# Optimization experiments

Measured on AMD Instinct MI355X. Metric: run time of the kernel, lower is better.

The kernel has to match this reference:

```python
import jax, jax.numpy as jnp
import numpy as np

C64 = jnp.complex64

# ---- gate matrices (PennyLane conventions) ----

def u3(theta, phi, delta):
    ct, st = jnp.cos(theta / 2), jnp.sin(theta / 2)
    return jnp.stack([
        jnp.stack([ct + 0j, -jnp.exp(1j * delta) * st]),
        jnp.stack([jnp.exp(1j * phi) * st, jnp.exp(1j * (phi + delta)) * ct]),
    ]).astype(C64)

def ising_zz(t):
    em, ep = jnp.exp(-1j * t / 2), jnp.exp(1j * t / 2)
    return jnp.diag(jnp.stack([em, ep, ep, em])).astype(C64)

_XX = np.fliplr(np.eye(4)).astype(np.complex64)
_YY = np.array([[0, 0, 0, -1], [0, 0, 1, 0], [0, 1, 0, 0], [-1, 0, 0, 0]], np.complex64)
_I4 = np.eye(4, dtype=np.complex64)

def ising_xx(t):
    return (jnp.cos(t / 2) * _I4 - 1j * jnp.sin(t / 2) * _XX).astype(C64)

def ising_yy(t):
    return (jnp.cos(t / 2) * _I4 - 1j * jnp.sin(t / 2) * _YY).astype(C64)

def crot(phi, theta, omega):
    # controlled-Rot(phi,theta,omega); control = first wire of apply_2q
    ct, st = jnp.cos(theta / 2), jnp.sin(theta / 2)
    r = jnp.stack([
        jnp.stack([jnp.exp(-1j * (phi + omega) / 2) * ct, -jnp.exp(1j * (phi - omega) / 2) * st]),
        jnp.stack([jnp.exp(-1j * (phi - omega) / 2) * st, jnp.exp(1j * (phi + omega) / 2) * ct]),
    ])
    U = jnp.eye(4, dtype=C64)
    return U.at[2:, 2:].set(r.astype(C64))

# ---- statevector gate application; state shape (S, 2, 2, ..., 2) (wire 0 = axis 1) ----

def apply_1q(state, U, q):
    st = jnp.tensordot(U, state, axes=[[1], [q + 1]])  # (2, S, ...)
    return jnp.moveaxis(st, 0, q + 1)

def apply_2q(state, U4, q1, q2):
    Ut = U4.reshape(2, 2, 2, 2)  # (o1, o2, i1, i2)
    st = jnp.tensordot(Ut, state, axes=[[2, 3], [q1 + 1, q2 + 1]])
    return jnp.moveaxis(st, [0, 1], [q1 + 1, q2 + 1])

KERNEL, DILATION = 8, 1

def setup_inputs() -> dict:
    key = jax.random.key(0)
    ks = jax.random.split(key, 5)
    B, C, T = 16, 32, 128
    nq, depth = 10, 3
    return {
        "x": jax.random.normal(ks[0], (B, C, T), jnp.float32),
        "fc_w": jax.random.normal(ks[1], (nq, C * KERNEL), jnp.float32) * (1.0 / np.sqrt(C * KERNEL)),
        "fc_b": jax.random.normal(ks[2], (nq,), jnp.float32) * 0.01,
        "conv_params": jax.random.normal(ks[3], (depth, nq, 15), jnp.float32),
        "pool_params": jax.random.normal(ks[4], (depth, nq // 2, 3), jnp.float32),
    }

def reference(x, fc_w, fc_b, conv_params, pool_params):
    B, C, T = x.shape
    nq = fc_w.shape[0]
    k = fc_w.shape[1] // C
    depth = conv_params.shape[0]
    d = DILATION
    n_win = T - (k - 1) * d

    # temporal windows -> classical embedding (angles)
    idx = jnp.arange(n_win)[:, None] + d * jnp.arange(k)[None, :]  # (n_win, k)
    win = x[:, :, idx]                                             # (B, C, n_win, k)
    flat = jnp.transpose(win, (0, 2, 1, 3)).reshape(B, n_win, C * k)
    angles = (jnp.einsum('bwf,ef->bwe', flat, fc_w) + fc_b).reshape(-1, nq)  # (S, nq)
    S = angles.shape[0]

    # AngleEmbedding with RY on |0...0> gives a product state
    half = angles / 2
    c, s = jnp.cos(half), jnp.sin(half)
    state = jnp.ones((S, 1), C64)
    for q in range(nq):
        qubit = jnp.stack([c[:, q], s[:, q]], axis=-1).astype(C64)  # (S, 2)
        state = (state[:, :, None] * qubit[:, None, :]).reshape(S, -1)
    state = state.reshape((S,) + (2,) * nq)

    wires = list(range(nq))
    for layer in range(depth):
        W = conv_params[layer]
        P = pool_params[layer]
        nw = len(wires)
        # convolution: U3 pairs + IsingZZ/YY/XX + U3 pairs, even then odd brickwork
        for p in (0, 1):
            for indx in range(nw - 1):
                if indx % 2 == p:
                    w1, w2 = wires[indx], wires[indx + 1]
                    state = apply_1q(state, u3(*W[indx, 0:3]), w1)
                    state = apply_1q(state, u3(*W[indx + 1, 3:6]), w2)
                    state = apply_2q(state, ising_zz(W[indx, 6]), w1, w2)
                    state = apply_2q(state, ising_yy(W[indx, 7]), w1, w2)
                    state = apply_2q(state, ising_xx(W[indx, 8]), w1, w2)
                    state = apply_1q(state, u3(*W[indx, 9:12]), w1)
                    state = apply_1q(state, u3(*W[indx + 1, 12:15]), w2)
        # pooling: CRot from discarded (odd) wire onto kept (even) wire
        for j in range(nw // 2):
            ctrl, tgt = wires[2 * j + 1], wires[2 * j]
            state = apply_2q(state, crot(*P[j]), ctrl, tgt)
        wires = wires[::2]

    # expval(PauliZ(0))
    probs = state.real ** 2 + state.imag ** 2
    p01 = probs.reshape(S, 2, -1).sum(-1)  # marginal over wire 0
    z = p01[:, 0] - p01[:, 1]
    return z.reshape(B, n_win)
```

## Files before the change

kernel.cpp:

```cpp
#include <hip/hip_runtime.h>

#define NWIN 121
#define NQ 10
#define NGATES 23
#define WPB 4

typedef float v2f __attribute__((ext_vector_type(2)));

__device__ static const int dGT[NGATES] = {0,0,0,0,0,0,0,0,0, 1,1,1,1,1, 0,0,0,0, 1,1, 0,0, 1};
__device__ static const int dGL[NGATES] = {0,0,0,0,0,0,0,0,0, 0,0,0,0,0, 1,1,1,1, 1,1, 2,2, 2};
__device__ static const int dGP[NGATES] = {0,2,4,6,8,1,3,5,7, 0,1,2,3,4, 0,2,1,3, 0,1, 0,1, 0};

__host__ __device__ constexpr int REGB[4][4] = {
    {5,6,7,8},{1,2,3,4},{0,1,3,5},{3,5,7,9}};
__host__ __device__ constexpr int LANEB[4][6] = {
    {0,1,2,3,4,9},{0,5,6,7,8,9},{2,4,6,7,8,9},{0,1,2,4,6,8}};

__host__ __device__ constexpr int hswz(int p, int L){
    return p==0 ? ((((L>>5)&1)<<1)|(((L>>6)&1)<<2)|(((L>>7)&1)<<3))
         : p==1 ? (((L>>4)&1) | ((((L>>5)&1)^((L>>6)&1))<<1) | (((L>>7)&1)<<2) | (((L>>8)&1)<<3))
         :        (((L>>4)&1) | (((L>>6)&1)<<1) | (((L>>8)&1)<<3));
}
__host__ __device__ constexpr int offsL(int ph, int r){
    int o = 0;
    for (int k=0;k<4;++k) if ((r>>k)&1) o |= 1<<REGB[ph][k];
    return o;
}

struct cpx { float x, y; };
__device__ __forceinline__ cpx cmul(cpx a, cpx b){ return {a.x*b.x - a.y*b.y, a.x*b.y + a.y*b.x}; }
__device__ __forceinline__ cpx cadd(cpx a, cpx b){ return {a.x+b.x, a.y+b.y}; }
__device__ __forceinline__ cpx cscale(float s, cpx a){ return {s*a.x, s*a.y}; }
__device__ __forceinline__ cpx cexp_i(float t){ return {cosf(t), sinf(t)}; }
__device__ __forceinline__ cpx mulnegi(cpx z){ return {z.y, -z.x}; }
__device__ __forceinline__ cpx csel(int c, cpx a, cpx b){ return {c ? a.x : b.x, c ? a.y : b.y}; }

__device__ __forceinline__ void u3m(cpx A[2][2], float th, float ph, float de){
    float ct = cosf(0.5f*th), st = sinf(0.5f*th);
    cpx ed  = cexp_i(de);
    cpx ep  = cexp_i(ph);
    cpx epd = cexp_i(ph + de);
    A[0][0] = {ct, 0.f};
    A[0][1] = {-ed.x*st, -ed.y*st};
    A[1][0] = { ep.x*st,  ep.y*st};
    A[1][1] = { epd.x*ct, epd.y*ct};
}

__device__ __forceinline__ void build_gate_col(int g, int c,
                                               const float* __restrict__ conv,
                                               const float* __restrict__ pool,
                                               cpx (&Mc)[4])
{
    int l = dGL[g], pi = dGP[g];
    if (dGT[g] == 0) {
        const float* W1 = conv + l*150 + pi*15;
        const float* W2 = conv + l*150 + (pi+1)*15;
        cpx A1[2][2], B1[2][2], A2[2][2], B2[2][2];
        u3m(A1, W1[0],  W1[1],  W1[2]);
        u3m(B1, W2[3],  W2[4],  W2[5]);
        u3m(A2, W1[9],  W1[10], W1[11]);
        u3m(B2, W2[12], W2[13], W2[14]);
        const int c1 = c >> 1, c2 = c & 1;
        cpx a1r0 = csel(c1, A1[0][1], A1[0][0]);
        cpx a1r1 = csel(c1, A1[1][1], A1[1][0]);
        cpx b1r0 = csel(c2, B1[0][1], B1[0][0]);
        cpx b1r1 = csel(c2, B1[1][1], B1[1][0]);
        cpx T[4];
        T[0] = cmul(a1r0, b1r0);
        T[1] = cmul(a1r0, b1r1);
        T[2] = cmul(a1r1, b1r0);
        T[3] = cmul(a1r1, b1r1);
        float tz = W1[6];
        cpx em = cexp_i(-0.5f*tz), ep = cexp_i(0.5f*tz);
        T[0] = cmul(em, T[0]); T[1] = cmul(ep, T[1]);
        T[2] = cmul(ep, T[2]); T[3] = cmul(em, T[3]);
        float ty = W1[7]; float cy = cosf(0.5f*ty), sy = sinf(0.5f*ty);
        cpx T2_[4];
        T2_[0] = cadd(cscale(cy,T[0]), mulnegi(cscale(-sy, T[3])));
        T2_[1] = cadd(cscale(cy,T[1]), mulnegi(cscale( sy, T[2])));
        T2_[2] = cadd(cscale(cy,T[2]), mulnegi(cscale( sy, T[1])));
        T2_[3] = cadd(cscale(cy,T[3]), mulnegi(cscale(-sy, T[0])));
        float tx = W1[8]; float cx = cosf(0.5f*tx), sx = sinf(0.5f*tx);
        cpx T3_[4];
        T3_[0] = cadd(cscale(cx,T2_[0]), mulnegi(cscale(sx, T2_[3])));
        T3_[1] = cadd(cscale(cx,T2_[1]), mulnegi(cscale(sx, T2_[2])));
        T3_[2] = cadd(cscale(cx,T2_[2]), mulnegi(cscale(sx, T2_[1])));
        T3_[3] = cadd(cscale(cx,T2_[3]), mulnegi(cscale(sx, T2_[0])));
        cpx K2[4][4];
        #pragma unroll
        for (int r1=0;r1<2;++r1)
        #pragma unroll
        for (int r2=0;r2<2;++r2)
        #pragma unroll
        for (int d1=0;d1<2;++d1)
        #pragma unroll
        for (int d2=0;d2<2;++d2)
            K2[2*r1+r2][2*d1+d2] = cmul(A2[r1][d1], B2[r2][d2]);
        #pragma unroll
        for (int r=0;r<4;++r) {
            cpx acc = {0.f, 0.f};
            #pragma unroll
            for (int m=0;m<4;++m) acc = cadd(acc, cmul(K2[r][m], T3_[m]));
            Mc[r] = acc;
        }
    } else {
        const float* Pp = pool + l*15 + pi*3;
        float phi = Pp[0], th = Pp[1], om = Pp[2];
        float ct = cosf(0.5f*th), st = sinf(0.5f*th);
        cpx z = {0.f, 0.f}, one = {1.f, 0.f};
        cpx m22 = cscale( ct, cexp_i(-0.5f*(phi+om)));
        cpx m32 = cscale( st, cexp_i(-0.5f*(phi-om)));
        cpx m23 = cscale(-st, cexp_i( 0.5f*(phi-om)));
        cpx m33 = cscale( ct, cexp_i( 0.5f*(phi+om)));
        Mc[0] = csel(c == 0, one, z);
        Mc[1] = csel(c == 1, one, z);
        Mc[2] = csel(c == 2, m22, csel(c == 3, m23, z));
        Mc[3] = csel(c == 2, m32, csel(c == 3, m33, z));
    }
}


__device__ __forceinline__ v2f cfma(v2f m, v2f v, v2f acc) {
    v2f sw = {v.y, v.x};
    v2f my = {-m.y, m.y};
    v2f t = __builtin_elementwise_fma(my, sw, acc);
    v2f mx = {m.x, m.x};
    return __builtin_elementwise_fma(mx, v, t);
}
__device__ __forceinline__ v2f cmulv(v2f a, v2f b) { return cfma(a, b, (v2f){0.f,0.f}); }
__device__ __forceinline__ v2f vsel(int c, v2f a, v2f b) {
    return (v2f){ c ? a.x : b.x, c ? a.y : b.y };
}

__device__ __forceinline__ void wave_lds_fence() {
    asm volatile("s_waitcnt lgkmcnt(0)" ::: "memory");
}

template<int P1, int P2>
__device__ __forceinline__ void gate4(v2f (&st)[16], const float2* __restrict__ g) {
    v2f m[16];
    const float4* g4 = reinterpret_cast<const float4*>(g);
    #pragma unroll
    for (int k = 0; k < 8; ++k) {
        float4 t = g4[k];
        m[2*k]   = (v2f){t.x, t.y};
        m[2*k+1] = (v2f){t.z, t.w};
    }
    constexpr int M1 = 1 << P1, M2 = 1 << P2;
    #pragma unroll
    for (int b = 0; b < 16; ++b) {
        if (b & (M1 | M2)) continue;
        v2f v0 = st[b], v1 = st[b|M2], v2 = st[b|M1], v3 = st[b|M1|M2];
        #pragma unroll
        for (int row = 0; row < 4; ++row) {
            v2f acc = cfma(m[row*4+0], v0, (v2f){0.f, 0.f});
            acc = cfma(m[row*4+1], v1, acc);
            acc = cfma(m[row*4+2], v2, acc);
            acc = cfma(m[row*4+3], v3, acc);
            st[b | ((row>>1) ? M1 : 0) | ((row&1) ? M2 : 0)] = acc;
        }
    }
}

template<int P1, int P2>
__device__ __forceinline__ void crot4(v2f (&st)[16], const float2* __restrict__ g) {
    const float4* g4 = reinterpret_cast<const float4*>(g);
    float4 a = g4[5], bb = g4[7];
    v2f m22 = {a.x,a.y}, m23 = {a.z,a.w}, m32 = {bb.x,bb.y}, m33 = {bb.z,bb.w};
    constexpr int M1 = 1 << P1, M2 = 1 << P2;
    #pragma unroll
    for (int b = 0; b < 16; ++b) {
        if (!(b & M1) || (b & M2)) continue;
        v2f v2_ = st[b], v3_ = st[b|M2];
        st[b]    = cfma(m23, v3_, cmulv(m22, v2_));
        st[b|M2] = cfma(m33, v3_, cmulv(m32, v2_));
    }
}

template<int PCTRL, int LBIT>
__device__ __forceinline__ void crotx(v2f (&st)[16], const float2* __restrict__ g, int lane) {
    const float4* g4 = reinterpret_cast<const float4*>(g);
    float4 a = g4[5], bb = g4[7];
    v2f m22 = {a.x,a.y}, m23 = {a.z,a.w}, m32 = {bb.x,bb.y}, m33 = {bb.z,bb.w};
    const int beta = (lane >> LBIT) & 1;
    v2f S0 = vsel(beta, m33, m22);
    v2f S1 = vsel(beta, m32, m23);
    constexpr int M1 = 1 << PCTRL;
    #pragma unroll
    for (int b = 0; b < 16; ++b) {
        if (!(b & M1)) continue;
        v2f u = st[b], p;
        p.x = __shfl_xor(u.x, 1 << LBIT);
        p.y = __shfl_xor(u.y, 1 << LBIT);
        st[b] = cfma(S1, p, cmulv(S0, u));
    }
}

template<int PREG, int LBIT>
__device__ __forceinline__ void gate4x(v2f (&st)[16], const float2* __restrict__ g, int lane) {
    v2f m[16];
    const float4* g4 = reinterpret_cast<const float4*>(g);
    #pragma unroll
    for (int k = 0; k < 8; ++k) {
        float4 t = g4[k];
        m[2*k]   = (v2f){t.x, t.y};
        m[2*k+1] = (v2f){t.z, t.w};
    }
    const int beta = (lane >> LBIT) & 1;
    v2f A00 = vsel(beta, m[5],  m[0]);
    v2f A01 = vsel(beta, m[4],  m[1]);
    v2f A02 = vsel(beta, m[7],  m[2]);
    v2f A03 = vsel(beta, m[6],  m[3]);
    v2f A10 = vsel(beta, m[13], m[8]);
    v2f A11 = vsel(beta, m[12], m[9]);
    v2f A12 = vsel(beta, m[15], m[10]);
    v2f A13 = vsel(beta, m[14], m[11]);
    constexpr int M1 = 1 << PREG;
    #pragma unroll
    for (int b = 0; b < 16; ++b) {
        if (b & M1) continue;
        v2f u0 = st[b], u1 = st[b|M1], p0, p1;
        p0.x = __shfl_xor(u0.x, 1 << LBIT); p0.y = __shfl_xor(u0.y, 1 << LBIT);
        p1.x = __shfl_xor(u1.x, 1 << LBIT); p1.y = __shfl_xor(u1.y, 1 << LBIT);
        v2f r0 = cfma(A03, p1, cfma(A02, u1, cfma(A01, p0, cmulv(A00, u0))));
        v2f r1 = cfma(A13, p1, cfma(A12, u1, cfma(A11, p0, cmulv(A10, u0))));
        st[b] = r0; st[b|M1] = r1;
    }
}

template<int PH>
__device__ __forceinline__ int base_of(int lane) {
    int b = 0;
    #pragma unroll
    for (int j = 0; j < 6; ++j) b |= ((lane >> j) & 1) << LANEB[PH][j];
    return b;
}

template<int P>
__device__ __forceinline__ void permute(v2f (&st)[16], char* buf, int lane) {
    int bw0 = base_of<P>(lane);
    int bw = (bw0 ^ hswz(P, bw0)) << 3;
    #pragma unroll
    for (int r = 0; r < 16; ++r) {
        const int o = offsL(P, r);
        const int C = (o ^ hswz(P, o)) << 3;
        *reinterpret_cast<v2f*>(buf + (bw ^ C)) = st[r];
    }
    wave_lds_fence();
    int br0 = base_of<P+1>(lane);
    int br = (br0 ^ hswz(P, br0)) << 3;
    #pragma unroll
    for (int r = 0; r < 16; ++r) {
        const int o = offsL(P+1, r);
        const int C = (o ^ hswz(P, o)) << 3;
        st[r] = *reinterpret_cast<const v2f*>(buf + (br ^ C));
    }
}

__global__ __launch_bounds__(256, 2) void hqtcn_fused(
    const float* __restrict__ x,
    const float* __restrict__ fc_w,
    const float* __restrict__ fc_b,
    const float* __restrict__ conv,
    const float* __restrict__ pool,
    float* __restrict__ out)
{
    __shared__ float2 gmat[NGATES*16];
    __shared__ float2 pbuf[WPB][2][1024];

    const int tid  = threadIdx.x;
    const int wid  = tid >> 6;
    const int lane = tid & 63;
    const int s = blockIdx.x * WPB + wid;
    const int b = s / NWIN, w = s % NWIN;

    float xv[4];
    #pragma unroll
    for (int j = 0; j < 4; ++j) {
        int f = lane + 64*j;
        xv[j] = x[b*4096 + (f >> 3)*128 + w + (f & 7)];
    }

    if (tid < 4*NGATES) {
        cpx Mc[4];
        build_gate_col(tid >> 2, tid & 3, conv, pool, Mc);
        #pragma unroll
        for (int r = 0; r < 4; ++r)
            gmat[(tid>>2)*16 + r*4 + (tid&3)] = make_float2(Mc[r].x, Mc[r].y);
    }

    float cq[NQ], sq[NQ];
    #pragma unroll
    for (int e = 0; e < NQ; ++e) {
        float v = 0.f;
        #pragma unroll
        for (int j = 0; j < 4; ++j)
            v = fmaf(xv[j], fc_w[e*256 + lane + 64*j], v);
        #pragma unroll
        for (int off = 32; off >= 1; off >>= 1) v += __shfl_xor(v, off);
        float h = 0.5f * (v + fc_b[e]);
        __sincosf(h, &sq[e], &cq[e]);
    }
    __syncthreads();

    v2f W[5][4];
    #pragma unroll
    for (int p = 0; p < 5; ++p) {
        float ca = cq[2*p], sa = sq[2*p], cb = cq[2*p+1], sb = sq[2*p+1];
        float u0 = ca*cb, u1 = ca*sb, u2 = sa*cb, u3_ = sa*sb;
        const float2* G = gmat + p*16;
        #pragma unroll
        for (int i = 0; i < 4; ++i) {
            float2 g0 = G[i*4+0], g1 = G[i*4+1], g2 = G[i*4+2], g3 = G[i*4+3];
            v2f acc = (v2f){g0.x*u0, g0.y*u0};
            acc = __builtin_elementwise_fma((v2f){u1,u1}, (v2f){g1.x,g1.y}, acc);
            acc = __builtin_elementwise_fma((v2f){u2,u2}, (v2f){g2.x,g2.y}, acc);
            acc = __builtin_elementwise_fma((v2f){u3_,u3_}, (v2f){g3.x,g3.y}, acc);
            W[p][i] = acc;
        }
    }
    const int l0 = lane&1, l1=(lane>>1)&1, l2=(lane>>2)&1,
              l3=(lane>>3)&1, l4=(lane>>4)&1, l5=(lane>>5)&1;
    v2f W3k = vsel(l3, vsel(l2, W[3][3], W[3][2]), vsel(l2, W[3][1], W[3][0]));
    v2f W4k = vsel(l1, vsel(l0, W[4][3], W[4][2]), vsel(l0, W[4][1], W[4][0]));
    v2f UL  = cmulv(W3k, W4k);
    v2f W2lo = vsel(l4, W[2][1], W[2][0]);
    v2f W2hi = vsel(l4, W[2][3], W[2][2]);
    v2f P0v = cmulv(UL, vsel(l5, W[0][2], W[0][0]));
    v2f P1v = cmulv(UL, vsel(l5, W[0][3], W[0][1]));
    v2f PW[2][4];
    #pragma unroll
    for (int j = 0; j < 4; ++j) {
        PW[0][j] = cmulv(P0v, W[1][j]);
        PW[1][j] = cmulv(P1v, W[1][j]);
    }
    v2f st[16];
    #pragma unroll
    for (int r = 0; r < 16; ++r)
        st[r] = cmulv(PW[(r>>3)&1][(r>>1)&3], (r&1) ? W2hi : W2lo);

    const float2* gm = gmat;

    gate4<3,2>(st, gm + 5*16);
    gate4<1,0>(st, gm + 6*16);
    crot4<1,2>(st, gm + 10*16);
    crotx<3,5>(st, gm + 9*16, lane);
    permute<0>(st, (char*)&pbuf[wid][0][0], lane);
    gate4<3,2>(st, gm + 7*16);
    gate4<1,0>(st, gm + 8*16);
    crot4<1,2>(st, gm + 12*16);
    crotx<3,1>(st, gm + 11*16, lane);
    permute<1>(st, (char*)&pbuf[wid][1][0], lane);
    crot4<0,1>(st, gm + 13*16);
    gate4<3,2>(st, gm + 15*16);
    gate4<2,1>(st, gm + 17*16);
    permute<2>(st, (char*)&pbuf[wid][0][0], lane);
    gate4<3,2>(st, gm + 14*16);
    gate4<2,1>(st, gm + 16*16);
    crot4<2,3>(st, gm + 18*16);
    crot4<0,1>(st, gm + 19*16);
    gate4<3,1>(st, gm + 20*16);
    gate4x<1,1>(st, gm + 21*16, lane);
    crot4<1,3>(st, gm + 22*16);

    float accp = 0.f, accm = 0.f;
    #pragma unroll
    for (int r = 0; r < 16; ++r) {
        v2f a = st[r];
        float p2 = fmaf(a.x, a.x, a.y*a.y);
        if ((r >> 3) & 1) accm += p2; else accp += p2;
    }
    float acc = accp - accm;
    #pragma unroll
    for (int off = 32; off >= 1; off >>= 1) acc += __shfl_xor(acc, off);
    if (lane == 0) out[s] = acc;
}

extern "C" void kernel_launch(void* const* d_in, const int* in_sizes, int n_in,
                              void* d_out, int out_size, void* d_ws, size_t ws_size,
                              hipStream_t stream) {
    const float* x     = (const float*)d_in[0];
    const float* fc_w  = (const float*)d_in[1];
    const float* fc_b  = (const float*)d_in[2];
    const float* convp = (const float*)d_in[3];
    const float* poolp = (const float*)d_in[4];
    float* out = (float*)d_out;

    hqtcn_fused<<<(16*NWIN)/WPB, 64*WPB, 0, stream>>>(x, fc_w, fc_b, convp, poolp, out);
}
```

Measured before the change: 24.74 us.

## Split each 1024-amplitude statevector across two waves with 8 registers per lane

Each sample's 10-qubit state is now held by two wavefronts (8 amplitudes per lane instead of 16), with a new qubit-to-lane/register mapping. Gates are applied through register-register, register-lane and lane-lane variants that use cross-lane shuffles, and the three LDS permutes are replaced by a single block-level exchange behind __syncthreads. Grid doubles to two samples per 256-thread block, and launch bounds rise to four blocks per CU for more occupancy. In exchange there are more shuffle-heavy gates, an extra block barrier and a shared-memory reduction of the two partial expectations.

```diff
diff --git a/kernel.cpp b/kernel.cpp
--- a/kernel.cpp
+++ b/kernel.cpp
@@ -3,29 +3,12 @@
 #define NWIN 121
 #define NQ 10
 #define NGATES 23
-#define WPB 4
 
 typedef float v2f __attribute__((ext_vector_type(2)));
 
 __device__ static const int dGT[NGATES] = {0,0,0,0,0,0,0,0,0, 1,1,1,1,1, 0,0,0,0, 1,1, 0,0, 1};
 __device__ static const int dGL[NGATES] = {0,0,0,0,0,0,0,0,0, 0,0,0,0,0, 1,1,1,1, 1,1, 2,2, 2};
 __device__ static const int dGP[NGATES] = {0,2,4,6,8,1,3,5,7, 0,1,2,3,4, 0,2,1,3, 0,1, 0,1, 0};
-
-__host__ __device__ constexpr int REGB[4][4] = {
-    {5,6,7,8},{1,2,3,4},{0,1,3,5},{3,5,7,9}};
-__host__ __device__ constexpr int LANEB[4][6] = {
-    {0,1,2,3,4,9},{0,5,6,7,8,9},{2,4,6,7,8,9},{0,1,2,4,6,8}};
-
-__host__ __device__ constexpr int hswz(int p, int L){
-    return p==0 ? ((((L>>5)&1)<<1)|(((L>>6)&1)<<2)|(((L>>7)&1)<<3))
-         : p==1 ? (((L>>4)&1) | ((((L>>5)&1)^((L>>6)&1))<<1) | (((L>>7)&1)<<2) | (((L>>8)&1)<<3))
-         :        (((L>>4)&1) | (((L>>6)&1)<<1) | (((L>>8)&1)<<3));
-}
-__host__ __device__ constexpr int offsL(int ph, int r){
-    int o = 0;
-    for (int k=0;k<4;++k) if ((r>>k)&1) o |= 1<<REGB[ph][k];
-    return o;
-}
 
 struct cpx { float x, y; };
 __device__ __forceinline__ cpx cmul(cpx a, cpx b){ return {a.x*b.x - a.y*b.y, a.x*b.y + a.y*b.x}; }
@@ -131,14 +114,11 @@
 __device__ __forceinline__ v2f vsel(int c, v2f a, v2f b) {
     return (v2f){ c ? a.x : b.x, c ? a.y : b.y };
 }
-
-__device__ __forceinline__ void wave_lds_fence() {
-    asm volatile("s_waitcnt lgkmcnt(0)" ::: "memory");
-}
-
-template<int P1, int P2>
-__device__ __forceinline__ void gate4(v2f (&st)[16], const float2* __restrict__ g) {
-    v2f m[16];
+__device__ __forceinline__ v2f vshfl(v2f v, int m) {
+    return (v2f){ __shfl_xor(v.x, m), __shfl_xor(v.y, m) };
+}
+
+__device__ __forceinline__ void load16(const float2* __restrict__ g, v2f (&m)[16]) {
     const float4* g4 = reinterpret_cast<const float4*>(g);
     #pragma unroll
     for (int k = 0; k < 8; ++k) {
@@ -146,9 +126,20 @@
         m[2*k]   = (v2f){t.x, t.y};
         m[2*k+1] = (v2f){t.z, t.w};
     }
+}
+__device__ __forceinline__ void load4(const float2* __restrict__ g, v2f (&c4)[4]) {
+    const float4* g4 = reinterpret_cast<const float4*>(g);
+    float4 a = g4[5], b = g4[7];
+    c4[0] = (v2f){a.x,a.y}; c4[1] = (v2f){a.z,a.w};
+    c4[2] = (v2f){b.x,b.y}; c4[3] = (v2f){b.z,b.w};
+}
+
+template<int P1, int P2>
+__device__ __forceinline__ void gateRR(v2f (&st)[8], const float2* __restrict__ g) {
+    v2f m[16]; load16(g, m);
     constexpr int M1 = 1 << P1, M2 = 1 << P2;
     #pragma unroll
-    for (int b = 0; b < 16; ++b) {
+    for (int b = 0; b < 8; ++b) {
         if (b & (M1 | M2)) continue;
         v2f v0 = st[b], v1 = st[b|M2], v2 = st[b|M1], v3 = st[b|M1|M2];
         #pragma unroll
@@ -162,51 +153,10 @@
     }
 }
 
-template<int P1, int P2>
-__device__ __forceinline__ void crot4(v2f (&st)[16], const float2* __restrict__ g) {
-    const float4* g4 = reinterpret_cast<const float4*>(g);
-    float4 a = g4[5], bb = g4[7];
-    v2f m22 = {a.x,a.y}, m23 = {a.z,a.w}, m32 = {bb.x,bb.y}, m33 = {bb.z,bb.w};
-    constexpr int M1 = 1 << P1, M2 = 1 << P2;
-    #pragma unroll
-    for (int b = 0; b < 16; ++b) {
-        if (!(b & M1) || (b & M2)) continue;
-        v2f v2_ = st[b], v3_ = st[b|M2];
-        st[b]    = cfma(m23, v3_, cmulv(m22, v2_));
-        st[b|M2] = cfma(m33, v3_, cmulv(m32, v2_));
-    }
-}
-
-template<int PCTRL, int LBIT>
-__device__ __forceinline__ void crotx(v2f (&st)[16], const float2* __restrict__ g, int lane) {
-    const float4* g4 = reinterpret_cast<const float4*>(g);
-    float4 a = g4[5], bb = g4[7];
-    v2f m22 = {a.x,a.y}, m23 = {a.z,a.w}, m32 = {bb.x,bb.y}, m33 = {bb.z,bb.w};
-    const int beta = (lane >> LBIT) & 1;
-    v2f S0 = vsel(beta, m33, m22);
-    v2f S1 = vsel(beta, m32, m23);
-    constexpr int M1 = 1 << PCTRL;
-    #pragma unroll
-    for (int b = 0; b < 16; ++b) {
-        if (!(b & M1)) continue;
-        v2f u = st[b], p;
-        p.x = __shfl_xor(u.x, 1 << LBIT);
-        p.y = __shfl_xor(u.y, 1 << LBIT);
-        st[b] = cfma(S1, p, cmulv(S0, u));
-    }
-}
-
-template<int PREG, int LBIT>
-__device__ __forceinline__ void gate4x(v2f (&st)[16], const float2* __restrict__ g, int lane) {
-    v2f m[16];
-    const float4* g4 = reinterpret_cast<const float4*>(g);
-    #pragma unroll
-    for (int k = 0; k < 8; ++k) {
-        float4 t = g4[k];
-        m[2*k]   = (v2f){t.x, t.y};
-        m[2*k+1] = (v2f){t.z, t.w};
-    }
-    const int beta = (lane >> LBIT) & 1;
+template<int PREG, int LM>
+__device__ __forceinline__ void gateRL(v2f (&st)[8], const float2* __restrict__ g, int lane) {
+    v2f m[16]; load16(g, m);
+    const int beta = (lane & LM) ? 1 : 0;
     v2f A00 = vsel(beta, m[5],  m[0]);
     v2f A01 = vsel(beta, m[4],  m[1]);
     v2f A02 = vsel(beta, m[7],  m[2]);
@@ -217,47 +167,83 @@
     v2f A13 = vsel(beta, m[14], m[11]);
     constexpr int M1 = 1 << PREG;
     #pragma unroll
-    for (int b = 0; b < 16; ++b) {
+    for (int b = 0; b < 8; ++b) {
         if (b & M1) continue;
-        v2f u0 = st[b], u1 = st[b|M1], p0, p1;
-        p0.x = __shfl_xor(u0.x, 1 << LBIT); p0.y = __shfl_xor(u0.y, 1 << LBIT);
-        p1.x = __shfl_xor(u1.x, 1 << LBIT); p1.y = __shfl_xor(u1.y, 1 << LBIT);
+        v2f u0 = st[b], u1 = st[b|M1];
+        v2f p0 = vshfl(u0, LM), p1 = vshfl(u1, LM);
         v2f r0 = cfma(A03, p1, cfma(A02, u1, cfma(A01, p0, cmulv(A00, u0))));
         v2f r1 = cfma(A13, p1, cfma(A12, u1, cfma(A11, p0, cmulv(A10, u0))));
         st[b] = r0; st[b|M1] = r1;
     }
 }
 
-template<int PH>
-__device__ __forceinline__ int base_of(int lane) {
-    int b = 0;
-    #pragma unroll
-    for (int j = 0; j < 6; ++j) b |= ((lane >> j) & 1) << LANEB[PH][j];
-    return b;
-}
-
-template<int P>
-__device__ __forceinline__ void permute(v2f (&st)[16], char* buf, int lane) {
-    int bw0 = base_of<P>(lane);
-    int bw = (bw0 ^ hswz(P, bw0)) << 3;
-    #pragma unroll
-    for (int r = 0; r < 16; ++r) {
-        const int o = offsL(P, r);
-        const int C = (o ^ hswz(P, o)) << 3;
-        *reinterpret_cast<v2f*>(buf + (bw ^ C)) = st[r];
-    }
-    wave_lds_fence();
-    int br0 = base_of<P+1>(lane);
-    int br = (br0 ^ hswz(P, br0)) << 3;
-    #pragma unroll
-    for (int r = 0; r < 16; ++r) {
-        const int o = offsL(P+1, r);
-        const int C = (o ^ hswz(P, o)) << 3;
-        st[r] = *reinterpret_cast<const v2f*>(buf + (br ^ C));
-    }
-}
-
-__global__ __launch_bounds__(256, 2) void hqtcn_fused(
+template<int M1L, int M2L>
+__device__ __forceinline__ void gateLL(v2f (&st)[8], const float2* __restrict__ g, int lane) {
+    v2f m[16]; load16(g, m);
+    const int kb1 = (lane & M1L) ? 1 : 0;
+    const int kb0 = (lane & M2L) ? 1 : 0;
+    v2f C0 = vsel(kb1, vsel(kb0, m[15], m[10]), vsel(kb0, m[5],  m[0]));
+    v2f C1 = vsel(kb1, vsel(kb0, m[14], m[11]), vsel(kb0, m[4],  m[1]));
+    v2f C2 = vsel(kb1, vsel(kb0, m[13], m[8]),  vsel(kb0, m[7],  m[2]));
+    v2f C3 = vsel(kb1, vsel(kb0, m[12], m[9]),  vsel(kb0, m[6],  m[3]));
+    #pragma unroll
+    for (int r = 0; r < 8; ++r) {
+        v2f u  = st[r];
+        v2f q1 = vshfl(u, M2L);
+        v2f q2 = vshfl(u, M1L);
+        v2f q3 = vshfl(u, M1L | M2L);
+        st[r] = cfma(C3, q3, cfma(C2, q2, cfma(C1, q1, cmulv(C0, u))));
+    }
+}
+
+template<int CTRL, int TGT>
+__device__ __forceinline__ void crotRR(v2f (&st)[8], const float2* __restrict__ g) {
+    v2f c4[4]; load4(g, c4);
+    constexpr int MC = 1 << CTRL, MT = 1 << TGT;
+    #pragma unroll
+    for (int b = 0; b < 8; ++b) {
+        if (!(b & MC) || (b & MT)) continue;
+        v2f v2_ = st[b], v3_ = st[b|MT];
+        st[b]    = cfma(c4[1], v3_, cmulv(c4[0], v2_));
+        st[b|MT] = cfma(c4[3], v3_, cmulv(c4[2], v2_));
+    }
+}
+
+template<int CM, int TR>
+__device__ __forceinline__ void crotLR(v2f (&st)[8], const float2* __restrict__ g, int lane) {
+    v2f c4[4]; load4(g, c4);
+    const int beta = (lane & CM) ? 1 : 0;
+    const v2f one = {1.f, 0.f}, zero = {0.f, 0.f};
+    v2f c00 = vsel(beta, c4[0], one);
+    v2f c01 = vsel(beta, c4[1], zero);
+    v2f c10 = vsel(beta, c4[2], zero);
+    v2f c11 = vsel(beta, c4[3], one);
+    constexpr int MT = 1 << TR;
+    #pragma unroll
+    for (int b = 0; b < 8; ++b) {
+        if (b & MT) continue;
+        v2f u = st[b], v = st[b|MT];
+        st[b]    = cfma(c01, v, cmulv(c00, u));
+        st[b|MT] = cfma(c11, v, cmulv(c10, u));
+    }
+}
+
+template<int CM, int TM>
+__device__ __forceinline__ void crotLL(v2f (&st)[8], const float2* __restrict__ g, int lane) {
+    v2f c4[4]; load4(g, c4);
+    const int ctl = (lane & CM) ? 1 : 0;
+    const int tgt = (lane & TM) ? 1 : 0;
+    const v2f one = {1.f, 0.f}, zero = {0.f, 0.f};
+    v2f c0 = vsel(ctl, vsel(tgt, c4[3], c4[0]), one);
+    v2f c1 = vsel(ctl, vsel(tgt, c4[2], c4[1]), zero);
+    #pragma unroll
+    for (int r = 0; r < 8; ++r) {
+        v2f p = vshfl(st[r], TM);
+        st[r] = cfma(c1, p, cmulv(c0, st[r]));
+    }
+}
+
+__global__ __launch_bounds__(256, 4) void hqtcn_fused(
     const float* __restrict__ x,
     const float* __restrict__ fc_w,
     const float* __restrict__ fc_b,
@@ -266,12 +252,15 @@
     float* __restrict__ out)
 {
     __shared__ float2 gmat[NGATES*16];
-    __shared__ float2 pbuf[WPB][2][1024];
+    __shared__ float2 pbuf[2][1024];
+    __shared__ float  red[2][2];
 
     const int tid  = threadIdx.x;
     const int wid  = tid >> 6;
     const int lane = tid & 63;
-    const int s = blockIdx.x * WPB + wid;
+    const int ws = wid >> 1;
+    const int wh = wid & 1;
+    const int s = blockIdx.x * 2 + ws;
     const int b = s / NWIN, w = s % NWIN;
 
     float xv[4];
@@ -303,7 +292,7 @@
     }
     __syncthreads();
 
-    v2f W[5][4];
+    v2f Wv[5][4];
     #pragma unroll
     for (int p = 0; p < 5; ++p) {
         float ca = cq[2*p], sa = sq[2*p], cb = cq[2*p+1], sb = sq[2*p+1];
@@ -316,64 +305,76 @@
             acc = __builtin_elementwise_fma((v2f){u1,u1}, (v2f){g1.x,g1.y}, acc);
             acc = __builtin_elementwise_fma((v2f){u2,u2}, (v2f){g2.x,g2.y}, acc);
             acc = __builtin_elementwise_fma((v2f){u3_,u3_}, (v2f){g3.x,g3.y}, acc);
-            W[p][i] = acc;
+            Wv[p][i] = acc;
         }
     }
     const int l0 = lane&1, l1=(lane>>1)&1, l2=(lane>>2)&1,
               l3=(lane>>3)&1, l4=(lane>>4)&1, l5=(lane>>5)&1;
-    v2f W3k = vsel(l3, vsel(l2, W[3][3], W[3][2]), vsel(l2, W[3][1], W[3][0]));
-    v2f W4k = vsel(l1, vsel(l0, W[4][3], W[4][2]), vsel(l0, W[4][1], W[4][0]));
-    v2f UL  = cmulv(W3k, W4k);
-    v2f W2lo = vsel(l4, W[2][1], W[2][0]);
-    v2f W2hi = vsel(l4, W[2][3], W[2][2]);
-    v2f P0v = cmulv(UL, vsel(l5, W[0][2], W[0][0]));
-    v2f P1v = cmulv(UL, vsel(l5, W[0][3], W[0][1]));
-    v2f PW[2][4];
-    #pragma unroll
-    for (int j = 0; j < 4; ++j) {
-        PW[0][j] = cmulv(P0v, W[1][j]);
-        PW[1][j] = cmulv(P1v, W[1][j]);
-    }
-    v2f st[16];
-    #pragma unroll
-    for (int r = 0; r < 16; ++r)
-        st[r] = cmulv(PW[(r>>3)&1][(r>>1)&3], (r&1) ? W2hi : W2lo);
+    v2f W2v = vsel(l5, vsel(l3, Wv[2][3], Wv[2][2]), vsel(l3, Wv[2][1], Wv[2][0]));
+    v2f W3v = vsel(l2, vsel(l1, Wv[3][3], Wv[3][2]), vsel(l1, Wv[3][1], Wv[3][0]));
+    v2f W4v = vsel(l0, vsel(l4, Wv[4][3], Wv[4][2]), vsel(l4, Wv[4][1], Wv[4][0]));
+    v2f A  = cmulv(W2v, cmulv(W3v, W4v));
+    v2f G0 = cmulv(A, vsel(wh, Wv[0][2], Wv[0][0]));
+    v2f G1 = cmulv(A, vsel(wh, Wv[0][3], Wv[0][1]));
+    v2f st[8];
+    #pragma unroll
+    for (int r = 0; r < 8; ++r) {
+        v2f D = Wv[1][2*((r>>1)&1) + (r&1)];
+        st[r] = cmulv((r >> 2) ? G1 : G0, D);
+    }
 
     const float2* gm = gmat;
 
-    gate4<3,2>(st, gm + 5*16);
-    gate4<1,0>(st, gm + 6*16);
-    crot4<1,2>(st, gm + 10*16);
-    crotx<3,5>(st, gm + 9*16, lane);
-    permute<0>(st, (char*)&pbuf[wid][0][0], lane);
-    gate4<3,2>(st, gm + 7*16);
-    gate4<1,0>(st, gm + 8*16);
-    crot4<1,2>(st, gm + 12*16);
-    crotx<3,1>(st, gm + 11*16, lane);
-    permute<1>(st, (char*)&pbuf[wid][1][0], lane);
-    crot4<0,1>(st, gm + 13*16);
-    gate4<3,2>(st, gm + 15*16);
-    gate4<2,1>(st, gm + 17*16);
-    permute<2>(st, (char*)&pbuf[wid][0][0], lane);
-    gate4<3,2>(st, gm + 14*16);
-    gate4<2,1>(st, gm + 16*16);
-    crot4<2,3>(st, gm + 18*16);
-    crot4<0,1>(st, gm + 19*16);
-    gate4<3,1>(st, gm + 20*16);
-    gate4x<1,1>(st, gm + 21*16, lane);
-    crot4<1,3>(st, gm + 22*16);
+    gateRR<2,1>(st, gm + 5*16);
+    gateRL<0,32>(st, gm + 6*16, lane);
+    gateLL<8,4>(st, gm + 7*16, lane);
+    gateLL<2,1>(st, gm + 8*16, lane);
+    crotRR<0,1>(st, gm + 10*16);
+    crotLL<8,32>(st, gm + 11*16, lane);
+    crotLL<2,4>(st, gm + 12*16, lane);
+    crotLL<16,1>(st, gm + 13*16, lane);
+
+    {
+        char* buf = (char*)&pbuf[ws][0];
+        const int bw = l4 | (l0<<1) | (l1<<2) | (l2<<3) | (l3<<4) | (l5<<5) | (wh<<9);
+        #pragma unroll
+        for (int r = 0; r < 8; ++r) {
+            int slot = (bw | ((r&1)<<6) | (((r>>1)&1)<<7) | (((r>>2)&1)<<8)) ^ ((r>>2)&1);
+            *reinterpret_cast<v2f*>(buf + (slot<<3)) = st[r];
+        }
+        __syncthreads();
+        const int br = (wh | (l1<<1) | (l3<<2) | (l0<<3) | (l4<<4) | (l5<<6) | (l2<<8)) ^ l2;
+        #pragma unroll
+        for (int r = 0; r < 8; ++r) {
+            int slot = br | ((r&1)<<5) | (((r>>1)&1)<<7) | (((r>>2)&1)<<9);
+            st[r] = *reinterpret_cast<const v2f*>(buf + (slot<<3));
+        }
+    }
+
+    crotLR<4,2>(st, gm + 9*16, lane);
+    gateRR<2,1>(st, gm + 14*16);
+    gateRL<0,1>(st, gm + 15*16, lane);
+    gateRR<1,0>(st, gm + 16*16);
+    gateLL<1,2>(st, gm + 17*16, lane);
+    crotRR<1,2>(st, gm + 18*16);
+    crotLR<1,0>(st, gm + 19*16, lane);
+    gateRR<2,0>(st, gm + 20*16);
+    gateRL<0,2>(st, gm + 21*16, lane);
+    crotRR<0,2>(st, gm + 22*16);
 
     float accp = 0.f, accm = 0.f;
     #pragma unroll
-    for (int r = 0; r < 16; ++r) {
+    for (int r = 0; r < 8; ++r) {
         v2f a = st[r];
         float p2 = fmaf(a.x, a.x, a.y*a.y);
-        if ((r >> 3) & 1) accm += p2; else accp += p2;
+        if (r & 4) accm += p2; else accp += p2;
     }
     float acc = accp - accm;
     #pragma unroll
     for (int off = 32; off >= 1; off >>= 1) acc += __shfl_xor(acc, off);
-    if (lane == 0) out[s] = acc;
+    if (lane == 0) red[ws][wh] = acc;
+    __syncthreads();
+    if (wh == 0 && lane == 0) out[s] = red[ws][0] + red[ws][1];
 }
 
 extern "C" void kernel_launch(void* const* d_in, const int* in_sizes, int n_in,
@@ -386,5 +387,5 @@
     const float* poolp = (const float*)d_in[4];
     float* out = (float*)d_out;
 
-    hqtcn_fused<<<(16*NWIN)/WPB, 64*WPB, 0, stream>>>(x, fc_w, fc_b, convp, poolp, out);
-}
+    hqtcn_fused<<<(16*NWIN)/2, 256, 0, stream>>>(x, fc_w, fc_b, convp, poolp, out);
+}
```

New measurement: 32.90 us. 33.0% more time.

## Software-pipeline gate matrix LDS loads and vectorize fc weight loads

Applied to the files above, without the earlier changes.

Gate matrices are now loaded from shared memory into double-buffered registers one or two gates ahead of their use, so LDS latency can overlap with the complex FMA work of the current gate. The window feature indexing changes to 4 consecutive elements per lane, which lets each lane read fc_w as one float4 instead of four strided scalar loads. The cost is higher register pressure from holding two 16-entry matrices at once, which may reduce occupancy. The permute barriers (lgkmcnt waits) may also force the prefetched loads to complete early, limiting how much overlap is actually gained.

```diff
diff --git a/kernel.cpp b/kernel.cpp
--- a/kernel.cpp
+++ b/kernel.cpp
@@ -136,9 +136,7 @@
     asm volatile("s_waitcnt lgkmcnt(0)" ::: "memory");
 }
 
-template<int P1, int P2>
-__device__ __forceinline__ void gate4(v2f (&st)[16], const float2* __restrict__ g) {
-    v2f m[16];
+__device__ __forceinline__ void load16(const float2* __restrict__ g, v2f (&m)[16]) {
     const float4* g4 = reinterpret_cast<const float4*>(g);
     #pragma unroll
     for (int k = 0; k < 8; ++k) {
@@ -146,6 +144,16 @@
         m[2*k]   = (v2f){t.x, t.y};
         m[2*k+1] = (v2f){t.z, t.w};
     }
+}
+__device__ __forceinline__ void load4(const float2* __restrict__ g, v2f (&c4)[4]) {
+    const float4* g4 = reinterpret_cast<const float4*>(g);
+    float4 a = g4[5], b = g4[7];
+    c4[0] = (v2f){a.x,a.y}; c4[1] = (v2f){a.z,a.w};
+    c4[2] = (v2f){b.x,b.y}; c4[3] = (v2f){b.z,b.w};
+}
+
+template<int P1, int P2>
+__device__ __forceinline__ void gate4m(v2f (&st)[16], const v2f (&m)[16]) {
     constexpr int M1 = 1 << P1, M2 = 1 << P2;
     #pragma unroll
     for (int b = 0; b < 16; ++b) {
@@ -163,28 +171,22 @@
 }
 
 template<int P1, int P2>
-__device__ __forceinline__ void crot4(v2f (&st)[16], const float2* __restrict__ g) {
-    const float4* g4 = reinterpret_cast<const float4*>(g);
-    float4 a = g4[5], bb = g4[7];
-    v2f m22 = {a.x,a.y}, m23 = {a.z,a.w}, m32 = {bb.x,bb.y}, m33 = {bb.z,bb.w};
+__device__ __forceinline__ void crot4m(v2f (&st)[16], const v2f (&c4)[4]) {
     constexpr int M1 = 1 << P1, M2 = 1 << P2;
     #pragma unroll
     for (int b = 0; b < 16; ++b) {
         if (!(b & M1) || (b & M2)) continue;
         v2f v2_ = st[b], v3_ = st[b|M2];
-        st[b]    = cfma(m23, v3_, cmulv(m22, v2_));
-        st[b|M2] = cfma(m33, v3_, cmulv(m32, v2_));
+        st[b]    = cfma(c4[1], v3_, cmulv(c4[0], v2_));
+        st[b|M2] = cfma(c4[3], v3_, cmulv(c4[2], v2_));
     }
 }
 
 template<int PCTRL, int LBIT>
-__device__ __forceinline__ void crotx(v2f (&st)[16], const float2* __restrict__ g, int lane) {
-    const float4* g4 = reinterpret_cast<const float4*>(g);
-    float4 a = g4[5], bb = g4[7];
-    v2f m22 = {a.x,a.y}, m23 = {a.z,a.w}, m32 = {bb.x,bb.y}, m33 = {bb.z,bb.w};
+__device__ __forceinline__ void crotxm(v2f (&st)[16], const v2f (&c4)[4], int lane) {
     const int beta = (lane >> LBIT) & 1;
-    v2f S0 = vsel(beta, m33, m22);
-    v2f S1 = vsel(beta, m32, m23);
+    v2f S0 = vsel(beta, c4[3], c4[0]);
+    v2f S1 = vsel(beta, c4[2], c4[1]);
     constexpr int M1 = 1 << PCTRL;
     #pragma unroll
     for (int b = 0; b < 16; ++b) {
@@ -197,15 +199,7 @@
 }
 
 template<int PREG, int LBIT>
-__device__ __forceinline__ void gate4x(v2f (&st)[16], const float2* __restrict__ g, int lane) {
-    v2f m[16];
-    const float4* g4 = reinterpret_cast<const float4*>(g);
-    #pragma unroll
-    for (int k = 0; k < 8; ++k) {
-        float4 t = g4[k];
-        m[2*k]   = (v2f){t.x, t.y};
-        m[2*k+1] = (v2f){t.z, t.w};
-    }
+__device__ __forceinline__ void gate4xm(v2f (&st)[16], const v2f (&m)[16], int lane) {
     const int beta = (lane >> LBIT) & 1;
     v2f A00 = vsel(beta, m[5],  m[0]);
     v2f A01 = vsel(beta, m[4],  m[1]);
@@ -277,7 +271,7 @@
     float xv[4];
     #pragma unroll
     for (int j = 0; j < 4; ++j) {
-        int f = lane + 64*j;
+        int f = 4*lane + j;
         xv[j] = x[b*4096 + (f >> 3)*128 + w + (f & 7)];
     }
 
@@ -292,10 +286,8 @@
     float cq[NQ], sq[NQ];
     #pragma unroll
     for (int e = 0; e < NQ; ++e) {
-        float v = 0.f;
-        #pragma unroll
-        for (int j = 0; j < 4; ++j)
-            v = fmaf(xv[j], fc_w[e*256 + lane + 64*j], v);
+        float4 wv = *reinterpret_cast<const float4*>(fc_w + e*256 + 4*lane);
+        float v = fmaf(xv[0], wv.x, fmaf(xv[1], wv.y, fmaf(xv[2], wv.z, xv[3]*wv.w)));
         #pragma unroll
         for (int off = 32; off >= 1; off >>= 1) v += __shfl_xor(v, off);
         float h = 0.5f * (v + fc_b[e]);
@@ -340,28 +332,45 @@
         st[r] = cmulv(PW[(r>>3)&1][(r>>1)&3], (r&1) ? W2hi : W2lo);
 
     const float2* gm = gmat;
-
-    gate4<3,2>(st, gm + 5*16);
-    gate4<1,0>(st, gm + 6*16);
-    crot4<1,2>(st, gm + 10*16);
-    crotx<3,5>(st, gm + 9*16, lane);
+    v2f mA[16], mB[16], cA[4], cB[4];
+
+    load16(gm + 5*16, mA); load16(gm + 6*16, mB);
+    load4 (gm + 10*16, cA); load4(gm + 9*16, cB);
+    gate4m<3,2>(st, mA);
+    load16(gm + 7*16, mA);
+    gate4m<1,0>(st, mB);
+    load16(gm + 8*16, mB);
+    crot4m<1,2>(st, cA);
+    load4(gm + 12*16, cA);
+    crotxm<3,5>(st, cB, lane);
+    load4(gm + 11*16, cB);
     permute<0>(st, (char*)&pbuf[wid][0][0], lane);
-    gate4<3,2>(st, gm + 7*16);
-    gate4<1,0>(st, gm + 8*16);
-    crot4<1,2>(st, gm + 12*16);
-    crotx<3,1>(st, gm + 11*16, lane);
+    gate4m<3,2>(st, mA);
+    load16(gm + 15*16, mA);
+    gate4m<1,0>(st, mB);
+    load16(gm + 17*16, mB);
+    crot4m<1,2>(st, cA);
+    load4(gm + 13*16, cA);
+    crotxm<3,1>(st, cB, lane);
     permute<1>(st, (char*)&pbuf[wid][1][0], lane);
-    crot4<0,1>(st, gm + 13*16);
-    gate4<3,2>(st, gm + 15*16);
-    gate4<2,1>(st, gm + 17*16);
+    crot4m<0,1>(st, cA);
+    load4(gm + 18*16, cA);
+    gate4m<3,2>(st, mA);
+    load16(gm + 14*16, mA);
+    gate4m<2,1>(st, mB);
+    load16(gm + 16*16, mB);
+    load4(gm + 19*16, cB);
     permute<2>(st, (char*)&pbuf[wid][0][0], lane);
-    gate4<3,2>(st, gm + 14*16);
-    gate4<2,1>(st, gm + 16*16);
-    crot4<2,3>(st, gm + 18*16);
-    crot4<0,1>(st, gm + 19*16);
-    gate4<3,1>(st, gm + 20*16);
-    gate4x<1,1>(st, gm + 21*16, lane);
-    crot4<1,3>(st, gm + 22*16);
+    gate4m<3,2>(st, mA);
+    load16(gm + 20*16, mA);
+    gate4m<2,1>(st, mB);
+    load16(gm + 21*16, mB);
+    crot4m<2,3>(st, cA);
+    load4(gm + 22*16, cA);
+    crot4m<0,1>(st, cB);
+    gate4m<3,1>(st, mA);
+    gate4xm<1,1>(st, mB, lane);
+    crot4m<1,3>(st, cA);
 
     float accp = 0.f, accm = 0.f;
     #pragma unroll
```

Result: no change. 24.65 us (-0.4%).
